# Performance work log

Hardware: AMD Instinct MI355X
Metric: run time of the kernel (lower is better)

The kernel has to match this reference:

```python
import jax, jax.numpy as jnp
import numpy as np
from jax import lax

B, C, IMG, PATCH = 128, 3, 224, 16
EMB, HEADS = 384, 6
NPATCH = (IMG // PATCH) ** 2          # 196
NTOK = NPATCH + 1                     # 197 (cls token)
HID = int(EMB * 4.0)                  # 1536 (also expert hidden)
NE, K = 4, 2                          # num_experts (hardcoded 4), top-k
NCLS = 1000


def _ln(x, g, b, eps=1e-5):
    m = jnp.mean(x, axis=-1, keepdims=True)
    v = jnp.mean((x - m) ** 2, axis=-1, keepdims=True)
    return (x - m) * lax.rsqrt(v + eps) * g + b


def setup_inputs() -> dict:
    key = jax.random.key(0)
    ks = jax.random.split(key, 16)
    s = 0.02
    return {
        "x": jax.random.normal(ks[0], (B, C, IMG, IMG), jnp.float32),
        "conv_w": jax.random.normal(ks[1], (EMB, C, PATCH, PATCH), jnp.float32) * s,
        "conv_b": jnp.zeros((EMB,), jnp.float32),
        "cls_token": jax.random.normal(ks[2], (1, 1, EMB), jnp.float32) * s,
        "pos_embed": jax.random.normal(ks[3], (1, NTOK, EMB), jnp.float32) * s,
        "ln1_g": jnp.ones((EMB,), jnp.float32),
        "ln1_b": jnp.zeros((EMB,), jnp.float32),
        "in_proj_w": jax.random.normal(ks[4], (3 * EMB, EMB), jnp.float32) * s,
        "in_proj_b": jnp.zeros((3 * EMB,), jnp.float32),
        "out_proj_w": jax.random.normal(ks[5], (EMB, EMB), jnp.float32) * s,
        "out_proj_b": jnp.zeros((EMB,), jnp.float32),
        "router_w": jax.random.normal(ks[6], (NE, EMB), jnp.float32) * s,
        "router_b": jnp.zeros((NE,), jnp.float32),
        "ew1": jax.random.normal(ks[7], (NE, EMB, HID), jnp.float32) * s,
        "eb1": jnp.zeros((NE, HID), jnp.float32),
        "ew2": jax.random.normal(ks[8], (NE, HID, EMB), jnp.float32) * s,
        "eb2": jnp.zeros((NE, EMB), jnp.float32),
        "ln2_g": jnp.ones((EMB,), jnp.float32),
        "ln2_b": jnp.zeros((EMB,), jnp.float32),
        "head_w": jax.random.normal(ks[9], (NCLS, EMB), jnp.float32) * s,
        "head_b": jnp.zeros((NCLS,), jnp.float32),
    }


def reference(x, conv_w, conv_b, cls_token, pos_embed,
              ln1_g, ln1_b, in_proj_w, in_proj_b, out_proj_w, out_proj_b,
              router_w, router_b, ew1, eb1, ew2, eb2,
              ln2_g, ln2_b, head_w, head_b):
    # ---- patch embedding: Conv2d(stride=kernel=patch) -> [B, N, E]
    h = lax.conv_general_dilated(x, conv_w, window_strides=(PATCH, PATCH),
                                 padding="VALID",
                                 dimension_numbers=("NCHW", "OIHW", "NCHW"))
    h = h + conv_b[None, :, None, None]
    h = h.reshape(B, EMB, NPATCH).transpose(0, 2, 1)          # [B, 196, E]
    h = jnp.concatenate([jnp.broadcast_to(cls_token, (B, 1, EMB)), h], axis=1)
    h = h + pos_embed                                         # [B, 197, E]

    # ---- SelfAttentionBlock (NOTE: no residual; same LN applied twice, as in source)
    hn = _ln(h, ln1_g, ln1_b)
    qkv = hn @ in_proj_w.T + in_proj_b                        # [B, N, 3E]
    q, k, v = jnp.split(qkv, 3, axis=-1)
    hd = EMB // HEADS
    q = q.reshape(B, NTOK, HEADS, hd)
    k = k.reshape(B, NTOK, HEADS, hd)
    v = v.reshape(B, NTOK, HEADS, hd)
    att = jnp.einsum("bqhd,bkhd->bhqk", q, k) / np.sqrt(hd).astype(np.float32)
    att = jax.nn.softmax(att, axis=-1)
    o = jnp.einsum("bhqk,bkhd->bqhd", att, v).reshape(B, NTOK, EMB)
    o = o @ out_proj_w.T + out_proj_b
    h = _ln(o, ln1_g, ln1_b)                                  # second LN, same params

    # ---- MoE: dense all-expert FFN + top-k gather + mean
    scores = jax.nn.softmax(h @ router_w.T + router_b, axis=-1)   # [B, N, NE]
    topk_vals, topk_idx = lax.top_k(scores, K)                    # [B, N, K]
    flat = h.reshape(B * NTOK, EMB)
    eh = jax.nn.gelu(jnp.einsum("te,neh->tnh", flat, ew1) + eb1, approximate=False)
    eo = jnp.einsum("tnh,nhe->tne", eh, ew2) + eb2                # [BN, NE, E]
    idx = topk_idx.reshape(B * NTOK, K, 1)
    sel = jnp.take_along_axis(eo, idx, axis=1)                    # [BN, K, E]
    h = sel.mean(axis=1).reshape(B, NTOK, EMB)

    # ---- final norm + classification head on cls token
    h = _ln(h, ln2_g, ln2_b)
    return h[:, 0] @ head_w.T + head_b                            # [B, NCLS]
```

## Files before the change

### kernel.cpp

```cpp
#include <hip/hip_runtime.h>
#include <cstdint>
#include <cstddef>

typedef _Float16 f16;
typedef _Float16 f16x2 __attribute__((ext_vector_type(2)));
typedef _Float16 f16x8 __attribute__((ext_vector_type(8)));
typedef float    f32x4 __attribute__((ext_vector_type(4)));

constexpr int NTOKC  = 197;
constexpr int TTOK   = 128 * 197;
constexpr int EMB    = 384;
constexpr int HID    = 1536;

constexpr size_t OFF_CONVW   = 0;
constexpr size_t OFF_EW1T    = 1179648;
constexpr size_t OFF_EW2T    = 5898240;
constexpr size_t OFF_HEADW16 = 10616832;
constexpr size_t OFF_XCLS16  = 11403264;
constexpr size_t OFF_Q       = 11404800;
constexpr size_t OFF_HCLS16  = 11799552;
constexpr size_t OFF_MASKW   = 11897856;
constexpr size_t OFF_EH      = 11899904;
constexpr size_t OFF_EPART   = 13472768;
constexpr size_t OFF_HFIN    = 16618496;
constexpr size_t OFF_XH      = 16716800;
constexpr size_t OFF_R       = 36082688;
constexpr size_t OFF_CVEC    = 36094976;
constexpr size_t OFF_U16     = 36099072;
constexpr size_t OFF_O16     = 36688896;
constexpr size_t OFF_WV16    = 36787200;
constexpr size_t OFF_WOUT16  = 37082112;
constexpr size_t OFF_O2CLS   = 37377024;
constexpr size_t OFF_P32     = 37573632;
constexpr size_t OFF_SG      = 38212608;
constexpr size_t OFF_SCLS    = 38817792;
constexpr size_t WS_NEEDED   = 38818816;

__device__ __forceinline__ void gload16(const void* g, void* l) {
  __builtin_amdgcn_global_load_lds(
      (__attribute__((address_space(1))) void*)(void*)g,
      (__attribute__((address_space(3))) void*)l, 16, 0, 0);
}

__global__ __launch_bounds__(256) void prep_cast_k(
    const float* __restrict__ conv_w, const float* __restrict__ head_w,
    const float* __restrict__ inp_w, const float* __restrict__ outp_w,
    f16* __restrict__ convw, f16* __restrict__ headw16,
    f16* __restrict__ wv16, f16* __restrict__ wout16) {
  int i = blockIdx.x * 256 + threadIdx.x;
  if (i < 294912) convw[i] = (f16)conv_w[i];
  int j = i - 294912;
  if (j >= 0 && j < 393216) {
    int row = j / 384;
    headw16[j] = (row < 1000) ? (f16)head_w[j] : (f16)0.f;
  }
  int k = i - 688128;
  if (k >= 0 && k < 147456) wv16[k] = (f16)inp_w[294912 + k];
  int l = i - 835584;
  if (l >= 0 && l < 147456) wout16[l] = (f16)outp_w[l];
}

__global__ __launch_bounds__(256) void transpose_cast_k(
    const float* __restrict__ in, f16* __restrict__ outp, int R, int C) {
  __shared__ float tile[32][33];
  int e = blockIdx.z;
  const float* pin = in + (size_t)e * R * C;
  f16* pout = outp + (size_t)e * R * C;
  int c0 = blockIdx.x * 32, r0 = blockIdx.y * 32;
  int tx = threadIdx.x & 31, ty = threadIdx.x >> 5;
#pragma unroll
  for (int i = 0; i < 4; i++)
    tile[ty + 8 * i][tx] = pin[(size_t)(r0 + ty + 8 * i) * C + c0 + tx];
  __syncthreads();
#pragma unroll
  for (int i = 0; i < 4; i++)
    pout[(size_t)(c0 + ty + 8 * i) * R + r0 + tx] = (f16)tile[tx][ty + 8 * i];
}

__global__ __launch_bounds__(384) void clsprep_k(
    const float* __restrict__ cls, const float* __restrict__ posw,
    const float* __restrict__ g, const float* __restrict__ bb,
    const float* __restrict__ Wq, const float* __restrict__ bq,
    f16* __restrict__ xcls16, float* __restrict__ qout) {
  __shared__ float xs[EMB];
  __shared__ float red[16];
  int t = threadIdx.x, lane = t & 63, wave = t >> 6;
  float v = cls[t] + posw[t];
  float s = v, sq = v * v;
#pragma unroll
  for (int off = 32; off; off >>= 1) {
    s += __shfl_xor(s, off);
    sq += __shfl_xor(sq, off);
  }
  if (lane == 0) { red[wave] = s; red[8 + wave] = sq; }
  __syncthreads();
  float S = 0.f, SQ = 0.f;
#pragma unroll
  for (int i = 0; i < 6; i++) { S += red[i]; SQ += red[8 + i]; }
  float m = S * (1.f / 384.f);
  float rs = rsqrtf(SQ * (1.f / 384.f) - m * m + 1e-5f);
  float y = (v - m) * rs * g[t] + bb[t];
  xs[t] = y;
  xcls16[t] = (f16)y;
  __syncthreads();
  const float4* w4 = (const float4*)(Wq + (size_t)t * EMB);
  const float4* s4 = (const float4*)xs;
  float a = bq[t];
#pragma unroll 8
  for (int i = 0; i < 96; i++) {
    float4 xx = s4[i], ww = w4[i];
    a += xx.x * ww.x + xx.y * ww.y + xx.z * ww.z + xx.w * ww.w;
  }
  qout[t] = a;
}

__global__ __launch_bounds__(384) void rprep_k(
    const float* __restrict__ inp_w, const float* __restrict__ inp_b,
    const float* __restrict__ qv, const f16* __restrict__ xcls16,
    float* __restrict__ Rg, float* __restrict__ Cg, float* __restrict__ Scls) {
  int h = blockIdx.x, t = threadIdx.x;
  __shared__ float qs[64];
  __shared__ float cred[64];
  __shared__ float sred[6];
  if (t < 64) {
    float q = qv[h * 64 + t];
    qs[t] = q;
    cred[t] = q * inp_b[384 + h * 64 + t];
  }
  __syncthreads();
  const float* wp = inp_w + ((size_t)(384 + h * 64)) * 384 + t;
  float a = 0.f;
#pragma unroll 8
  for (int d = 0; d < 64; d++) a += wp[(size_t)d * 384] * qs[d];
  Rg[h * 384 + t] = a;
  float part = a * (float)xcls16[t];
  int lane = t & 63, wave = t >> 6;
#pragma unroll
  for (int off = 32; off; off >>= 1) part += __shfl_xor(part, off);
  if (lane == 0) sred[wave] = part;
  __syncthreads();
  if (t == 0) {
    float c = 0.f;
    for (int d = 0; d < 64; d++) c += cred[d];
    Cg[h] = c;
    float stot = c;
#pragma unroll
    for (int i = 0; i < 6; i++) stot += sred[i];
    Scls[h] = stot;
  }
}

__global__ __launch_bounds__(384) void bcast_cls_k(
    const f16* __restrict__ xcls16, const float* __restrict__ Scls,
    f16* __restrict__ xh, float* __restrict__ Sg) {
  int b = blockIdx.x, t = threadIdx.x;
  xh[(size_t)b * NTOKC * EMB + t] = xcls16[t];
  if (t < 6) Sg[((size_t)b * 6 + t) * 197] = Scls[t];
}

__global__ __launch_bounds__(1024) void embed_ln_k(
    const float* __restrict__ img, const f16* __restrict__ B,
    const float* __restrict__ bias, const float* __restrict__ posw,
    const float* __restrict__ g, const float* __restrict__ bb,
    const float* __restrict__ Rg, const float* __restrict__ Cg,
    f16* __restrict__ xh, float* __restrict__ Sg) {
  __shared__ f16 As[64 * 32];
  __shared__ f16 Bs[384 * 32];
  __shared__ float prm[3 * 384];
  __shared__ float psum[64 * 4];
  __shared__ float pqsum[64 * 4];
  __shared__ float Rs2[2304];
  __shared__ float psc[64 * 24];
  const int K = 768;
  const int tid = threadIdx.x;
  const int lane = tid & 63;
  const int wave = tid >> 6;
  const int rowgrp = wave & 3;
  const int colgrp = wave >> 2;
  const int m0 = (int)blockIdx.x * 64;
  const int fr = lane & 15;
  const int fq = lane >> 4;

  for (int i = tid; i < 384; i += 1024) {
    prm[i] = bias[i]; prm[384 + i] = g[i]; prm[768 + i] = bb[i];
  }
  for (int i = tid; i < 2304; i += 1024) Rs2[i] = Rg[i];

  f32x4 acc[6];
#pragma unroll
  for (int j = 0; j < 6; j++) acc[j] = f32x4{0.f, 0.f, 0.f, 0.f};

  const int sr = lane >> 2, sc = (lane & 3) * 8;
  const float* abase = nullptr;
  f16* adst = nullptr;
  if (wave < 4) {
    int row = m0 + wave * 16 + sr;
    int bimg = row / 196;
    int pp = row - bimg * 196;
    int py = pp / 14, px = pp - py * 14;
    int kx0 = sc & 15;
    abase = img + ((size_t)(bimg * 3) * 224 + py * 16) * 224 + px * 16 + kx0;
    adst = As + (wave * 16 + sr) * 32 + sc;
  }
  const f16* gb0 = nullptr;
  f16* lb0 = nullptr;
  if (wave >= 4) {
    int brow = (wave - 4) * 32;
    gb0 = B + (size_t)(brow + sr) * K + sc;
    lb0 = Bs + brow * 32;
  }

  for (int k0 = 0; k0 < K; k0 += 32) {
    if (wave < 4) {
      int col = k0 + sc;
      int c = col >> 8;
      int ky = (col >> 4) & 15;
      const float* src = abase + c * 50176 + ky * 224;
      float4 p0 = *(const float4*)src;
      float4 p1 = *(const float4*)(src + 4);
      f16x8 hv;
      hv[0] = (f16)p0.x; hv[1] = (f16)p0.y; hv[2] = (f16)p0.z; hv[3] = (f16)p0.w;
      hv[4] = (f16)p1.x; hv[5] = (f16)p1.y; hv[6] = (f16)p1.z; hv[7] = (f16)p1.w;
      *(f16x8*)adst = hv;
    } else {
      gload16(gb0, lb0); gload16(gb0 + (size_t)16 * K, lb0 + 16 * 32);
      gb0 += 32;
    }
    __syncthreads();
    f16x8 af = *(const f16x8*)&As[(rowgrp * 16 + fr) * 32 + fq * 8];
#pragma unroll
    for (int j = 0; j < 6; j++) {
      f16x8 bf = *(const f16x8*)&Bs[(colgrp * 96 + j * 16 + fr) * 32 + fq * 8];
      acc[j] = __builtin_amdgcn_mfma_f32_16x16x32_f16(af, bf, acc[j], 0, 0, 0);
    }
    __syncthreads();
  }

  float v[4][6];
#pragma unroll
  for (int rg = 0; rg < 4; rg++) {
    int lrow = rowgrp * 16 + fq * 4 + rg;
    int row = m0 + lrow;
    int bimg = row / 196;
    int pp = row - bimg * 196;
    const float* prow = posw + (size_t)(pp + 1) * EMB;
    float s = 0.f, sq = 0.f;
#pragma unroll
    for (int j = 0; j < 6; j++) {
      int col = colgrp * 96 + j * 16 + fr;
      float t = acc[j][rg] + prm[col] + prow[col];
      v[rg][j] = t;
      s += t; sq += t * t;
    }
#pragma unroll
    for (int off = 1; off < 16; off <<= 1) {
      s += __shfl_xor(s, off);
      sq += __shfl_xor(sq, off);
    }
    if (fr == 0) { psum[lrow * 4 + colgrp] = s; pqsum[lrow * 4 + colgrp] = sq; }
  }
  __syncthreads();

#pragma unroll
  for (int rg = 0; rg < 4; rg++) {
    int lrow = rowgrp * 16 + fq * 4 + rg;
    float S = psum[lrow * 4] + psum[lrow * 4 + 1] + psum[lrow * 4 + 2] + psum[lrow * 4 + 3];
    float SQ = pqsum[lrow * 4] + pqsum[lrow * 4 + 1] + pqsum[lrow * 4 + 2] + pqsum[lrow * 4 + 3];
    float m = S * (1.f / 384.f);
    float rs = rsqrtf(SQ * (1.f / 384.f) - m * m + 1e-5f);
    int row = m0 + lrow;
    int bimg = row / 196;
    int pp = row - bimg * 196;
    f16* orow = xh + ((size_t)bimg * NTOKC + pp + 1) * EMB;
#pragma unroll
    for (int j = 0; j < 6; j++) {
      int col = colgrp * 96 + j * 16 + fr;
      float y = (v[rg][j] - m) * rs * prm[384 + col] + prm[768 + col];
      v[rg][j] = y;
      orow[col] = (f16)y;
    }
  }

#pragma unroll
  for (int h = 0; h < 6; h++) {
    float rv[6];
#pragma unroll
    for (int j = 0; j < 6; j++)
      rv[j] = Rs2[h * 384 + colgrp * 96 + j * 16 + fr];
#pragma unroll
    for (int rg = 0; rg < 4; rg++) {
      float p = v[rg][0] * rv[0] + v[rg][1] * rv[1] + v[rg][2] * rv[2]
              + v[rg][3] * rv[3] + v[rg][4] * rv[4] + v[rg][5] * rv[5];
#pragma unroll
      for (int off = 1; off < 16; off <<= 1) p += __shfl_xor(p, off);
      if (fr == 0) psc[(rowgrp * 16 + fq * 4 + rg) * 24 + colgrp * 6 + h] = p;
    }
  }
  __syncthreads();
  if (tid < 384) {
    int lrow = tid / 6, h = tid - lrow * 6;
    float s = psc[lrow * 24 + h] + psc[lrow * 24 + 6 + h]
            + psc[lrow * 24 + 12 + h] + psc[lrow * 24 + 18 + h] + Cg[h];
    int row = m0 + lrow;
    int bimg = row / 196, pp = row - bimg * 196;
    Sg[((size_t)bimg * 6 + h) * 197 + pp + 1] = s;
  }
}

__global__ __launch_bounds__(384) void softmax_k(
    const float* __restrict__ Sg, float* __restrict__ P32) {
  const int b = blockIdx.x, tid = threadIdx.x;
  const int wave = tid >> 6, lane = tid & 63;
  const float* sp = Sg + ((size_t)b * 6 + wave) * 197;
  float z[4], pk[4];
#pragma unroll
  for (int k = 0; k < 4; k++) {
    int t = lane + 64 * k;
    z[k] = (t < 197) ? sp[t] * 0.125f : -1e30f;
    pk[k] = 0.f;
  }
  float mx = fmaxf(fmaxf(z[0], z[1]), fmaxf(z[2], z[3]));
#pragma unroll
  for (int off = 32; off; off >>= 1) mx = fmaxf(mx, __shfl_xor(mx, off));
  float sum = 0.f;
#pragma unroll
  for (int k = 0; k < 4; k++) {
    int t = lane + 64 * k;
    if (t < 197) {
      pk[k] = __expf(z[k] - mx);
      sum += pk[k];
    }
  }
#pragma unroll
  for (int off = 32; off; off >>= 1) sum += __shfl_xor(sum, off);
  float si = 1.f / sum;
#pragma unroll
  for (int k = 0; k < 4; k++) {
    int t = lane + 64 * k;
    if (t < 208) P32[(size_t)b * 1248 + wave * 208 + t] = pk[k] * si;
  }
}

__global__ __launch_bounds__(256) void u_gemv_k(
    const float* __restrict__ P32, const f16* __restrict__ xh,
    f16* __restrict__ U16) {
  __shared__ float pf[6 * 208];
  __shared__ float part[4][64][12];
  const int cq = (int)blockIdx.x;
  const int b  = (int)blockIdx.y;
  const int tid = threadIdx.x;
  for (int i = tid; i < 1248; i += 256) pf[i] = P32[(size_t)b * 1248 + i];
  __syncthreads();
  const int cp = tid & 63;
  const int tq = tid >> 6;
  const int col0 = cq * 128 + cp * 2;
  const int t0 = 49 * tq;
  const int t1 = (tq == 3) ? 197 : t0 + 49;
  float acc[12];
#pragma unroll
  for (int r = 0; r < 12; r++) acc[r] = 0.f;
  const f16* xp = xh + ((size_t)b * NTOKC + t0) * EMB + col0;
#pragma unroll 2
  for (int t = t0; t < t1; t++) {
    f16x2 xv = *(const f16x2*)xp;
    float x0 = (float)xv[0];
    float x1 = (float)xv[1];
    xp += EMB;
#pragma unroll
    for (int h = 0; h < 6; h++) {
      float p = pf[h * 208 + t];
      acc[h * 2]     += p * x0;
      acc[h * 2 + 1] += p * x1;
    }
  }
#pragma unroll
  for (int r = 0; r < 12; r++) part[tq][cp][r] = acc[r];
  __syncthreads();
#pragma unroll
  for (int k = 0; k < 3; k++) {
    int idx = tid + k * 256;
    int cp2 = idx / 12, slot = idx - cp2 * 12;
    int h = slot >> 1, c01 = slot & 1;
    float u = part[0][cp2][slot] + part[1][cp2][slot] +
              part[2][cp2][slot] + part[3][cp2][slot];
    U16[(size_t)b * 2304 + h * 384 + cq * 128 + cp2 * 2 + c01] = (f16)u;
  }
}

__global__ __launch_bounds__(256) void vproj_k(
    const f16* __restrict__ U16, const f16* __restrict__ wv16,
    const float* __restrict__ inp_b, f16* __restrict__ O16) {
  __shared__ f16 As[128 * 32];
  __shared__ f16 Bs[64 * 32];
  const int tid = threadIdx.x;
  const int lane = tid & 63;
  const int wave = tid >> 6;
  const int h = (int)blockIdx.x;
  const int wm = (wave >> 1) * 64;
  const int wn = (wave & 1) * 32;
  const int fr = lane & 15;
  const int fq = lane >> 4;
  const float* bv = inp_b + 768 + h * 64;

  f32x4 acc[4][2];
#pragma unroll
  for (int i = 0; i < 4; i++)
#pragma unroll
    for (int j = 0; j < 2; j++) acc[i][j] = f32x4{0.f, 0.f, 0.f, 0.f};

  const int sr = lane >> 2;
  const int sc = (lane & 3) * 8;
  const f16* ag = U16 + (size_t)(wave * 32 + sr) * 2304 + h * 384 + sc;
  const f16* bg = wv16 + (size_t)(h * 64 + wave * 16 + sr) * 384 + sc;
  const size_t rstepA = (size_t)16 * 2304;
  f16* la = As + wave * 32 * 32;
  f16* lb = Bs + wave * 16 * 32;

  for (int k0 = 0; k0 < 384; k0 += 32) {
    gload16(ag, la);  gload16(ag + rstepA, la + 16 * 32);
    gload16(bg, lb);
    ag += 32; bg += 32;
    __syncthreads();
    f16x8 af[4], bf[2];
#pragma unroll
    for (int i = 0; i < 4; i++)
      af[i] = *(const f16x8*)&As[(wm + i * 16 + fr) * 32 + fq * 8];
#pragma unroll
    for (int j = 0; j < 2; j++)
      bf[j] = *(const f16x8*)&Bs[(wn + j * 16 + fr) * 32 + fq * 8];
#pragma unroll
    for (int i = 0; i < 4; i++)
#pragma unroll
      for (int j = 0; j < 2; j++)
        acc[i][j] = __builtin_amdgcn_mfma_f32_16x16x32_f16(af[i], bf[j], acc[i][j], 0, 0, 0);
    __syncthreads();
  }

#pragma unroll
  for (int i = 0; i < 4; i++)
#pragma unroll
    for (int j = 0; j < 2; j++)
#pragma unroll
      for (int rg = 0; rg < 4; rg++) {
        int gm = wm + i * 16 + fq * 4 + rg;
        int gn = wn + j * 16 + fr;
        O16[(size_t)gm * EMB + h * 64 + gn] = (f16)(acc[i][j][rg] + bv[gn]);
      }
}

__global__ __launch_bounds__(256) void oproj_k(
    const f16* __restrict__ O16, const f16* __restrict__ wout16,
    const float* __restrict__ bout, float* __restrict__ o2cls) {
  __shared__ f16 As[128 * 32];
  __shared__ f16 Bs[64 * 32];
  const int tid = threadIdx.x;
  const int lane = tid & 63;
  const int wave = tid >> 6;
  const int n0 = (int)blockIdx.x * 64;
  const int wm = (wave >> 1) * 64;
  const int wn = (wave & 1) * 32;
  const int fr = lane & 15;
  const int fq = lane >> 4;

  f32x4 acc[4][2];
#pragma unroll
  for (int i = 0; i < 4; i++)
#pragma unroll
    for (int j = 0; j < 2; j++) acc[i][j] = f32x4{0.f, 0.f, 0.f, 0.f};

  const int sr = lane >> 2;
  const int sc = (lane & 3) * 8;
  const f16* ag = O16 + (size_t)(wave * 32 + sr) * 384 + sc;
  const f16* bg = wout16 + (size_t)(n0 + wave * 16 + sr) * 384 + sc;
  const size_t rstep = (size_t)16 * 384;
  f16* la = As + wave * 32 * 32;
  f16* lb = Bs + wave * 16 * 32;

  for (int k0 = 0; k0 < 384; k0 += 32) {
    gload16(ag, la);  gload16(ag + rstep, la + 16 * 32);
    gload16(bg, lb);
    ag += 32; bg += 32;
    __syncthreads();
    f16x8 af[4], bf[2];
#pragma unroll
    for (int i = 0; i < 4; i++)
      af[i] = *(const f16x8*)&As[(wm + i * 16 + fr) * 32 + fq * 8];
#pragma unroll
    for (int j = 0; j < 2; j++)
      bf[j] = *(const f16x8*)&Bs[(wn + j * 16 + fr) * 32 + fq * 8];
#pragma unroll
    for (int i = 0; i < 4; i++)
#pragma unroll
      for (int j = 0; j < 2; j++)
        acc[i][j] = __builtin_amdgcn_mfma_f32_16x16x32_f16(af[i], bf[j], acc[i][j], 0, 0, 0);
    __syncthreads();
  }

#pragma unroll
  for (int i = 0; i < 4; i++)
#pragma unroll
    for (int j = 0; j < 2; j++)
#pragma unroll
      for (int rg = 0; rg < 4; rg++) {
        int gm = wm + i * 16 + fq * 4 + rg;
        int gn = n0 + wn + j * 16 + fr;
        o2cls[(size_t)gm * EMB + gn] = acc[i][j][rg] + bout[gn];
      }
}

__global__ __launch_bounds__(384) void ln_router_k(
    const float* __restrict__ o2cls, const float* __restrict__ g, const float* __restrict__ bb,
    const float* __restrict__ rw, const float* __restrict__ rb,
    f16* __restrict__ hcls16, float* __restrict__ maskw) {
  __shared__ float red[16];
  __shared__ float part[6][4];
  __shared__ float logits[4];
  int b = blockIdx.x, t = threadIdx.x;
  int lane = t & 63, wave = t >> 6;
  float v = o2cls[(size_t)b * EMB + t];
  float s = v, sq = v * v;
#pragma unroll
  for (int off = 32; off; off >>= 1) {
    s += __shfl_xor(s, off);
    sq += __shfl_xor(sq, off);
  }
  if (lane == 0) { red[wave] = s; red[8 + wave] = sq; }
  __syncthreads();
  float S = 0.f, SQ = 0.f;
#pragma unroll
  for (int i = 0; i < 6; i++) { S += red[i]; SQ += red[8 + i]; }
  float m = S * (1.f / 384.f);
  float rs = rsqrtf(SQ * (1.f / 384.f) - m * m + 1e-5f);
  float y = (v - m) * rs * g[t] + bb[t];
  hcls16[(size_t)b * EMB + t] = (f16)y;
  float p0 = y * rw[t];
  float p1 = y * rw[EMB + t];
  float p2 = y * rw[2 * EMB + t];
  float p3 = y * rw[3 * EMB + t];
#pragma unroll
  for (int off = 32; off; off >>= 1) {
    p0 += __shfl_xor(p0, off);
    p1 += __shfl_xor(p1, off);
    p2 += __shfl_xor(p2, off);
    p3 += __shfl_xor(p3, off);
  }
  if (lane == 0) { part[wave][0] = p0; part[wave][1] = p1; part[wave][2] = p2; part[wave][3] = p3; }
  __syncthreads();
  if (t < 4) {
    float a = rb[t];
#pragma unroll
    for (int i = 0; i < 6; i++) a += part[i][t];
    logits[t] = a;
  }
  __syncthreads();
  if (t == 0) {
    float l0 = logits[0], l1 = logits[1], l2 = logits[2], l3 = logits[3];
    int i1 = 0; float b1 = l0;
    if (l1 > b1) { b1 = l1; i1 = 1; }
    if (l2 > b1) { b1 = l2; i1 = 2; }
    if (l3 > b1) { b1 = l3; i1 = 3; }
    int i2 = -1; float b2 = 0.f;
    float lv[4] = {l0, l1, l2, l3};
#pragma unroll
    for (int i = 0; i < 4; i++) {
      if (i == i1) continue;
      if (i2 < 0 || lv[i] > b2) { i2 = i; b2 = lv[i]; }
    }
#pragma unroll
    for (int e = 0; e < 4; e++)
      maskw[(size_t)b * 4 + e] = (e == i1 || e == i2) ? 0.5f : 0.f;
  }
}

__global__ __launch_bounds__(256) void moe1_k(
    const f16* __restrict__ A, const f16* __restrict__ Bm,
    const float* __restrict__ bias, f16* __restrict__ outh) {
  __shared__ f16 As[128 * 32];
  __shared__ f16 Bs[64 * 32];
  const int K = EMB;
  const int tid = threadIdx.x;
  const int lane = tid & 63;
  const int wave = tid >> 6;
  const int e = (int)blockIdx.y;
  const int n0 = (int)blockIdx.x * 64;
  const int wm = (wave >> 1) * 64;
  const int wn = (wave & 1) * 32;
  const int fr = lane & 15;
  const int fq = lane >> 4;
  Bm += (size_t)e * HID * EMB;
  bias += (size_t)e * HID;

  f32x4 acc[4][2];
#pragma unroll
  for (int i = 0; i < 4; i++)
#pragma unroll
    for (int j = 0; j < 2; j++) acc[i][j] = f32x4{0.f, 0.f, 0.f, 0.f};

  const int sr = lane >> 2;
  const int sc = (lane & 3) * 8;
  const f16* ag = A + (size_t)(wave * 32 + sr) * K + sc;
  const f16* bg = Bm + (size_t)(n0 + wave * 16 + sr) * K + sc;
  const size_t rstep = (size_t)16 * K;
  f16* la = As + wave * 32 * 32;
  f16* lb = Bs + wave * 16 * 32;

  for (int k0 = 0; k0 < K; k0 += 32) {
    gload16(ag, la);  gload16(ag + rstep, la + 16 * 32);
    gload16(bg, lb);
    ag += 32; bg += 32;
    __syncthreads();
    f16x8 af[4], bf[2];
#pragma unroll
    for (int i = 0; i < 4; i++)
      af[i] = *(const f16x8*)&As[(wm + i * 16 + fr) * 32 + fq * 8];
#pragma unroll
    for (int j = 0; j < 2; j++)
      bf[j] = *(const f16x8*)&Bs[(wn + j * 16 + fr) * 32 + fq * 8];
#pragma unroll
    for (int i = 0; i < 4; i++)
#pragma unroll
      for (int j = 0; j < 2; j++)
        acc[i][j] = __builtin_amdgcn_mfma_f32_16x16x32_f16(af[i], bf[j], acc[i][j], 0, 0, 0);
    __syncthreads();
  }

#pragma unroll
  for (int i = 0; i < 4; i++)
#pragma unroll
    for (int j = 0; j < 2; j++)
#pragma unroll
      for (int rg = 0; rg < 4; rg++) {
        int gm = wm + i * 16 + fq * 4 + rg;
        int gn = n0 + wn + j * 16 + fr;
        float v = acc[i][j][rg] + bias[gn];
        float gl = 0.5f * v * (1.0f + erff(v * 0.70710678118654752f));
        outh[(size_t)e * 128 * HID + (size_t)gm * HID + gn] = (f16)gl;
      }
}

__global__ __launch_bounds__(256) void moe2_k(
    const f16* __restrict__ EH, const f16* __restrict__ W2,
    float* __restrict__ part) {
  __shared__ f16 As[128 * 32];
  __shared__ f16 Bs[64 * 32];
  const int tid = threadIdx.x;
  const int lane = tid & 63;
  const int wave = tid >> 6;
  const int n0 = (int)blockIdx.x * 64;
  const int e = (int)blockIdx.y;
  const int kc = (int)blockIdx.z;
  const int wm = (wave >> 1) * 64;
  const int wn = (wave & 1) * 32;
  const int fr = lane & 15;
  const int fq = lane >> 4;
  const f16* A = EH + (size_t)e * 128 * HID + kc * 384;
  const f16* B = W2 + (size_t)e * EMB * HID + kc * 384;

  f32x4 acc[4][2];
#pragma unroll
  for (int i = 0; i < 4; i++)
#pragma unroll
    for (int j = 0; j < 2; j++) acc[i][j] = f32x4{0.f, 0.f, 0.f, 0.f};

  const int sr = lane >> 2;
  const int sc = (lane & 3) * 8;
  const f16* ag = A + (size_t)(wave * 32 + sr) * HID + sc;
  const f16* bg = B + (size_t)(n0 + wave * 16 + sr) * HID + sc;
  const size_t rstep = (size_t)16 * HID;
  f16* la = As + wave * 32 * 32;
  f16* lb = Bs + wave * 16 * 32;

  for (int k0 = 0; k0 < 384; k0 += 32) {
    gload16(ag, la);  gload16(ag + rstep, la + 16 * 32);
    gload16(bg, lb);
    ag += 32; bg += 32;
    __syncthreads();
    f16x8 af[4], bf[2];
#pragma unroll
    for (int i = 0; i < 4; i++)
      af[i] = *(const f16x8*)&As[(wm + i * 16 + fr) * 32 + fq * 8];
#pragma unroll
    for (int j = 0; j < 2; j++)
      bf[j] = *(const f16x8*)&Bs[(wn + j * 16 + fr) * 32 + fq * 8];
#pragma unroll
    for (int i = 0; i < 4; i++)
#pragma unroll
      for (int j = 0; j < 2; j++)
        acc[i][j] = __builtin_amdgcn_mfma_f32_16x16x32_f16(af[i], bf[j], acc[i][j], 0, 0, 0);
    __syncthreads();
  }

#pragma unroll
  for (int i = 0; i < 4; i++)
#pragma unroll
    for (int j = 0; j < 2; j++)
#pragma unroll
      for (int rg = 0; rg < 4; rg++) {
        int gm = wm + i * 16 + fq * 4 + rg;
        int gn = n0 + wn + j * 16 + fr;
        part[(((size_t)kc * 4 + e) * 128 + gm) * EMB + gn] = acc[i][j][rg];
      }
}

__global__ __launch_bounds__(384) void combine_ln2_k(
    const float* __restrict__ part, const float* __restrict__ eb2,
    const float* __restrict__ maskw,
    const float* __restrict__ g, const float* __restrict__ bb,
    f16* __restrict__ hfin) {
  __shared__ float red[16];
  int b = blockIdx.x, t = threadIdx.x;
  int lane = t & 63, wave = t >> 6;
  float v = 0.f;
#pragma unroll
  for (int e = 0; e < 4; e++) {
    float s = eb2[e * EMB + t];
#pragma unroll
    for (int kc = 0; kc < 4; kc++)
      s += part[(((size_t)kc * 4 + e) * 128 + b) * EMB + t];
    v += maskw[b * 4 + e] * s;
  }
  float s = v, sq = v * v;
#pragma unroll
  for (int off = 32; off; off >>= 1) {
    s += __shfl_xor(s, off);
    sq += __shfl_xor(sq, off);
  }
  if (lane == 0) { red[wave] = s; red[8 + wave] = sq; }
  __syncthreads();
  float S = 0.f, SQ = 0.f;
#pragma unroll
  for (int i = 0; i < 6; i++) { S += red[i]; SQ += red[8 + i]; }
  float m = S * (1.f / 384.f);
  float rs = rsqrtf(SQ * (1.f / 384.f) - m * m + 1e-5f);
  hfin[(size_t)b * EMB + t] = (f16)((v - m) * rs * g[t] + bb[t]);
}

__global__ __launch_bounds__(256) void head_gemm_k(
    const f16* __restrict__ A, const f16* __restrict__ B,
    const float* __restrict__ hb, float* __restrict__ outp) {
  __shared__ f16 As[128 * 32];
  __shared__ f16 Bs[128 * 32];
  const int K = 384;
  const int tid = threadIdx.x;
  const int lane = tid & 63;
  const int wave = tid >> 6;
  const int n0 = (int)blockIdx.x * 128;
  const int wm = (wave >> 1) * 64;
  const int wn = (wave & 1) * 64;
  const int fr = lane & 15;
  const int fq = lane >> 4;

  f32x4 acc[4][4];
#pragma unroll
  for (int i = 0; i < 4; i++)
#pragma unroll
    for (int j = 0; j < 4; j++) acc[i][j] = f32x4{0.f, 0.f, 0.f, 0.f};

  const int srow = wave * 32 + (lane >> 2);
  const int scol = (lane & 3) * 8;
  const f16* ag = A + (size_t)srow * K + scol;
  const f16* bg = B + (size_t)(n0 + srow) * K + scol;
  const size_t rstep = (size_t)16 * K;
  f16* la = As + wave * 32 * 32;
  f16* lb = Bs + wave * 32 * 32;

  for (int k0 = 0; k0 < K; k0 += 32) {
    gload16(ag, la);          gload16(ag + rstep, la + 16 * 32);
    gload16(bg, lb);          gload16(bg + rstep, lb + 16 * 32);
    ag += 32; bg += 32;
    __syncthreads();
    f16x8 af[4], bf[4];
#pragma unroll
    for (int i = 0; i < 4; i++) {
      af[i] = *(const f16x8*)&As[(wm + i * 16 + fr) * 32 + fq * 8];
      bf[i] = *(const f16x8*)&Bs[(wn + i * 16 + fr) * 32 + fq * 8];
    }
#pragma unroll
    for (int i = 0; i < 4; i++)
#pragma unroll
      for (int j = 0; j < 4; j++)
        acc[i][j] = __builtin_amdgcn_mfma_f32_16x16x32_f16(af[i], bf[j], acc[i][j], 0, 0, 0);
    __syncthreads();
  }

#pragma unroll
  for (int i = 0; i < 4; i++)
#pragma unroll
    for (int j = 0; j < 4; j++)
#pragma unroll
      for (int rg = 0; rg < 4; rg++) {
        int gm = wm + i * 16 + fq * 4 + rg;
        int gn = n0 + wn + j * 16 + fr;
        if (gn < 1000)
          outp[(size_t)gm * 1000 + gn] = acc[i][j][rg] + hb[gn];
      }
}

extern "C" void kernel_launch(void* const* d_in, const int* in_sizes, int n_in,
                              void* d_out, int out_size, void* d_ws, size_t ws_size,
                              hipStream_t stream) {
  const float* x      = (const float*)d_in[0];
  const float* conv_w = (const float*)d_in[1];
  const float* conv_b = (const float*)d_in[2];
  const float* cls_t  = (const float*)d_in[3];
  const float* pos    = (const float*)d_in[4];
  const float* ln1_g  = (const float*)d_in[5];
  const float* ln1_b  = (const float*)d_in[6];
  const float* inp_w  = (const float*)d_in[7];
  const float* inp_b  = (const float*)d_in[8];
  const float* outp_w = (const float*)d_in[9];
  const float* outp_b = (const float*)d_in[10];
  const float* rt_w   = (const float*)d_in[11];
  const float* rt_b   = (const float*)d_in[12];
  const float* ew1    = (const float*)d_in[13];
  const float* eb1    = (const float*)d_in[14];
  const float* ew2    = (const float*)d_in[15];
  const float* eb2    = (const float*)d_in[16];
  const float* ln2_g  = (const float*)d_in[17];
  const float* ln2_b  = (const float*)d_in[18];
  const float* head_w = (const float*)d_in[19];
  const float* head_b = (const float*)d_in[20];
  float* out = (float*)d_out;
  char* w = (char*)d_ws;
  if (ws_size < WS_NEEDED) return;

  f16* convw    = (f16*)(w + OFF_CONVW);
  f16* ew1t     = (f16*)(w + OFF_EW1T);
  f16* ew2t     = (f16*)(w + OFF_EW2T);
  f16* headw16  = (f16*)(w + OFF_HEADW16);
  f16* xcls16   = (f16*)(w + OFF_XCLS16);
  float* qvec   = (float*)(w + OFF_Q);
  f16* hcls16   = (f16*)(w + OFF_HCLS16);
  float* maskw  = (float*)(w + OFF_MASKW);
  f16* ehbuf    = (f16*)(w + OFF_EH);
  float* epart  = (float*)(w + OFF_EPART);
  f16* hfin     = (f16*)(w + OFF_HFIN);
  f16* xh       = (f16*)(w + OFF_XH);
  float* Rg     = (float*)(w + OFF_R);
  float* Cg     = (float*)(w + OFF_CVEC);
  f16* u16      = (f16*)(w + OFF_U16);
  f16* o16      = (f16*)(w + OFF_O16);
  f16* wv16     = (f16*)(w + OFF_WV16);
  f16* wout16   = (f16*)(w + OFF_WOUT16);
  float* o2cls  = (float*)(w + OFF_O2CLS);
  float* p32    = (float*)(w + OFF_P32);
  float* sg     = (float*)(w + OFF_SG);
  float* scls   = (float*)(w + OFF_SCLS);

  prep_cast_k<<<dim3(3840), 256, 0, stream>>>(
      conv_w, head_w, inp_w, outp_w, convw, headw16, wv16, wout16);
  transpose_cast_k<<<dim3(48, 12, 4), 256, 0, stream>>>(ew1, ew1t, 384, 1536);
  transpose_cast_k<<<dim3(12, 48, 4), 256, 0, stream>>>(ew2, ew2t, 1536, 384);

  clsprep_k<<<dim3(1), 384, 0, stream>>>(cls_t, pos, ln1_g, ln1_b, inp_w, inp_b, xcls16, qvec);
  rprep_k<<<dim3(6), 384, 0, stream>>>(inp_w, inp_b, qvec, xcls16, Rg, Cg, scls);
  bcast_cls_k<<<dim3(128), 384, 0, stream>>>(xcls16, scls, xh, sg);

  embed_ln_k<<<dim3(392), 1024, 0, stream>>>(
      x, convw, conv_b, pos, ln1_g, ln1_b, Rg, Cg, xh, sg);

  softmax_k<<<dim3(128), 384, 0, stream>>>(sg, p32);
  u_gemv_k<<<dim3(3, 128), 256, 0, stream>>>(p32, xh, u16);
  vproj_k<<<dim3(6), 256, 0, stream>>>(u16, wv16, inp_b, o16);
  oproj_k<<<dim3(6), 256, 0, stream>>>(o16, wout16, outp_b, o2cls);
  ln_router_k<<<dim3(128), 384, 0, stream>>>(
      o2cls, ln1_g, ln1_b, rt_w, rt_b, hcls16, maskw);

  moe1_k<<<dim3(24, 4), 256, 0, stream>>>(hcls16, ew1t, eb1, ehbuf);
  moe2_k<<<dim3(6, 4, 4), 256, 0, stream>>>(ehbuf, ew2t, epart);
  combine_ln2_k<<<dim3(128), 384, 0, stream>>>(epart, eb2, maskw, ln2_g, ln2_b, hfin);

  head_gemm_k<<<dim3(8), 256, 0, stream>>>(hfin, headw16, head_b, out);
  (void)in_sizes; (void)n_in; (void)out_size;
}
```

Before: 344.5 us.

## Double-buffer patch-embed GEMM tiles and alias epilogue shared memory

New measurement: 321.7 us. 6.6% less time.

```diff
diff --git a/kernel.cpp b/kernel.cpp
--- a/kernel.cpp
+++ b/kernel.cpp
@@ -164,14 +164,13 @@
     const float* __restrict__ g, const float* __restrict__ bb,
     const float* __restrict__ Rg, const float* __restrict__ Cg,
     f16* __restrict__ xh, float* __restrict__ Sg) {
-  __shared__ f16 As[64 * 32];
-  __shared__ f16 Bs[384 * 32];
-  __shared__ float prm[3 * 384];
-  __shared__ float psum[64 * 4];
-  __shared__ float pqsum[64 * 4];
-  __shared__ float Rs2[2304];
-  __shared__ float psc[64 * 24];
+  __shared__ __attribute__((aligned(16))) char smem[57344];
+  f16* As0 = (f16*)smem;
+  f16* As1 = (f16*)(smem + 4096);
+  f16* Bs0 = (f16*)(smem + 8192);
+  f16* Bs1 = (f16*)(smem + 32768);
   const int K = 768;
+  const int NT = 24;
   const int tid = threadIdx.x;
   const int lane = tid & 63;
   const int wave = tid >> 6;
@@ -181,18 +180,13 @@
   const int fr = lane & 15;
   const int fq = lane >> 4;
 
-  for (int i = tid; i < 384; i += 1024) {
-    prm[i] = bias[i]; prm[384 + i] = g[i]; prm[768 + i] = bb[i];
-  }
-  for (int i = tid; i < 2304; i += 1024) Rs2[i] = Rg[i];
-
   f32x4 acc[6];
 #pragma unroll
   for (int j = 0; j < 6; j++) acc[j] = f32x4{0.f, 0.f, 0.f, 0.f};
 
   const int sr = lane >> 2, sc = (lane & 3) * 8;
   const float* abase = nullptr;
-  f16* adst = nullptr;
+  int adoff = 0;
   if (wave < 4) {
     int row = m0 + wave * 16 + sr;
     int bimg = row / 196;
@@ -200,41 +194,85 @@
     int py = pp / 14, px = pp - py * 14;
     int kx0 = sc & 15;
     abase = img + ((size_t)(bimg * 3) * 224 + py * 16) * 224 + px * 16 + kx0;
-    adst = As + (wave * 16 + sr) * 32 + sc;
+    adoff = (wave * 16 + sr) * 32 + sc;
   }
   const f16* gb0 = nullptr;
-  f16* lb0 = nullptr;
+  int lboff = 0;
   if (wave >= 4) {
     int brow = (wave - 4) * 32;
     gb0 = B + (size_t)(brow + sr) * K + sc;
-    lb0 = Bs + brow * 32;
-  }
-
-  for (int k0 = 0; k0 < K; k0 += 32) {
-    if (wave < 4) {
-      int col = k0 + sc;
-      int c = col >> 8;
-      int ky = (col >> 4) & 15;
-      const float* src = abase + c * 50176 + ky * 224;
+    lboff = brow * 32;
+  }
+
+  float4 n0, n1;
+  if (wave < 4) {
+    {
+      int col = sc;
+      const float* src = abase + (col >> 8) * 50176 + ((col >> 4) & 15) * 224;
       float4 p0 = *(const float4*)src;
       float4 p1 = *(const float4*)(src + 4);
       f16x8 hv;
       hv[0] = (f16)p0.x; hv[1] = (f16)p0.y; hv[2] = (f16)p0.z; hv[3] = (f16)p0.w;
       hv[4] = (f16)p1.x; hv[5] = (f16)p1.y; hv[6] = (f16)p1.z; hv[7] = (f16)p1.w;
-      *(f16x8*)adst = hv;
+      *(f16x8*)(As0 + adoff) = hv;
+    }
+    {
+      int col = 32 + sc;
+      const float* src = abase + (col >> 8) * 50176 + ((col >> 4) & 15) * 224;
+      n0 = *(const float4*)src;
+      n1 = *(const float4*)(src + 4);
+    }
+  } else {
+    gload16(gb0, Bs0 + lboff);
+    gload16(gb0 + (size_t)16 * K, Bs0 + lboff + 16 * 32);
+    gb0 += 32;
+  }
+  __syncthreads();
+
+  f16* AsC = As0; f16* AsN = As1;
+  f16* BsC = Bs0; f16* BsN = Bs1;
+
+  for (int t = 0; t < NT; ++t) {
+    if (wave < 4) {
+      if (t + 1 < NT) {
+        f16x8 hv;
+        hv[0] = (f16)n0.x; hv[1] = (f16)n0.y; hv[2] = (f16)n0.z; hv[3] = (f16)n0.w;
+        hv[4] = (f16)n1.x; hv[5] = (f16)n1.y; hv[6] = (f16)n1.z; hv[7] = (f16)n1.w;
+        *(f16x8*)(AsN + adoff) = hv;
+      }
+      if (t + 2 < NT) {
+        int col = (t + 2) * 32 + sc;
+        const float* src = abase + (col >> 8) * 50176 + ((col >> 4) & 15) * 224;
+        n0 = *(const float4*)src;
+        n1 = *(const float4*)(src + 4);
+      }
     } else {
-      gload16(gb0, lb0); gload16(gb0 + (size_t)16 * K, lb0 + 16 * 32);
-      gb0 += 32;
-    }
-    __syncthreads();
-    f16x8 af = *(const f16x8*)&As[(rowgrp * 16 + fr) * 32 + fq * 8];
+      if (t + 1 < NT) {
+        gload16(gb0, BsN + lboff);
+        gload16(gb0 + (size_t)16 * K, BsN + lboff + 16 * 32);
+        gb0 += 32;
+      }
+    }
+    f16x8 af = *(const f16x8*)&AsC[(rowgrp * 16 + fr) * 32 + fq * 8];
 #pragma unroll
     for (int j = 0; j < 6; j++) {
-      f16x8 bf = *(const f16x8*)&Bs[(colgrp * 96 + j * 16 + fr) * 32 + fq * 8];
+      f16x8 bf = *(const f16x8*)&BsC[(colgrp * 96 + j * 16 + fr) * 32 + fq * 8];
       acc[j] = __builtin_amdgcn_mfma_f32_16x16x32_f16(af, bf, acc[j], 0, 0, 0);
     }
     __syncthreads();
-  }
+    f16* tA = AsC; AsC = AsN; AsN = tA;
+    f16* tB = BsC; BsC = BsN; BsN = tB;
+  }
+
+  float* prm   = (float*)smem;
+  float* psum  = (float*)(smem + 4608);
+  float* pqsum = (float*)(smem + 5632);
+  float* Rs2   = (float*)(smem + 6656);
+  float* psc   = (float*)(smem + 15872);
+  for (int i = tid; i < 1152; i += 1024)
+    prm[i] = (i < 384) ? bias[i] : ((i < 768) ? g[i - 384] : bb[i - 768]);
+  for (int i = tid; i < 2304; i += 1024) Rs2[i] = Rg[i];
+  __syncthreads();
 
   float v[4][6];
 #pragma unroll
```
